# Kernel optimization log

Measured on AMD Instinct MI355X. Metric: run time of the kernel, lower is better.

The kernel has to match this reference:

```python
import jax, jax.numpy as jnp
import numpy as np

B, S, D = 2, 2048, 2048
H, HD = 16, 128
P = 2048  # past (cached) kv length


def setup_inputs() -> dict:
    key = jax.random.key(0)
    ks = jax.random.split(key, 12)
    sw = 1.0 / np.sqrt(D)
    inp = {
        "x": jax.random.normal(ks[0], (B, S, D), jnp.float32),
        "past_k": jax.random.normal(ks[1], (B, H, P, HD), jnp.float32),
        "past_v": jax.random.normal(ks[2], (B, H, P, HD), jnp.float32),
        "Wq": jax.random.normal(ks[3], (D, D), jnp.float32) * sw,
        "bq": jax.random.normal(ks[4], (D,), jnp.float32) * 0.01,
        "Wk": jax.random.normal(ks[5], (D, D), jnp.float32) * sw,
        "bk": jax.random.normal(ks[6], (D,), jnp.float32) * 0.01,
        "Wv": jax.random.normal(ks[7], (D, D), jnp.float32) * sw,
        "bv": jax.random.normal(ks[8], (D,), jnp.float32) * 0.01,
        "Wo": jax.random.normal(ks[9], (D, D), jnp.float32) * sw,
        "bo": jax.random.normal(ks[10], (D,), jnp.float32) * 0.01,
    }
    return inp


def _heads(t):
    # [B, S, D] -> [B, H, S, HD]
    return t.reshape(B, -1, H, HD).transpose(0, 2, 1, 3)


def reference(x, past_k, past_v, Wq, bq, Wk, bk, Wv, bv, Wo, bo):
    # QKV projections (separate weights, _qkv_same_embed_dim=False path)
    q = _heads(x @ Wq.T + bq)          # [B,H,S,HD]
    k_new = _heads(x @ Wk.T + bk)      # [B,H,S,HD]
    v_new = _heads(x @ Wv.T + bv)

    # KV cache append
    k_cached = jnp.concatenate([past_k, k_new], axis=2)  # [B,H,P+S,HD]
    v_cached = jnp.concatenate([past_v, v_new], axis=2)
    cached_len = P + S

    # Manual attention path (query_seq_len != cached_seq_len)
    scale = 1.0 / np.sqrt(HD)
    scores = jnp.einsum('bhqd,bhkd->bhqk', q, k_cached) * scale  # [B,H,S,P+S]
    q_pos = jnp.arange(cached_len - S, cached_len)[:, None]
    k_pos = jnp.arange(cached_len)[None, :]
    mask = q_pos >= k_pos  # offset causal mask [S, P+S]
    scores = jnp.where(mask, scores, -jnp.inf)
    attn = jax.nn.softmax(scores, axis=-1)
    out = jnp.einsum('bhqk,bhkd->bhqd', attn, v_cached)  # [B,H,S,HD]

    out = out.transpose(0, 2, 1, 3).reshape(B, S, D)
    return out @ Wo.T + bo
```

## Files before the change

kernel.cpp:

```cpp
#include <hip/hip_runtime.h>

typedef unsigned short u16;
typedef __attribute__((ext_vector_type(4))) float f32x4;
typedef __attribute__((ext_vector_type(16))) float f32x16;
typedef __attribute__((ext_vector_type(8))) short s16x8;
typedef __attribute__((ext_vector_type(2))) unsigned int u32x2v;

#define CEXP 0.12751742929f

static __device__ __forceinline__ u16 f2bf(float x) {
  unsigned u = __float_as_uint(x);
  u = u + 0x7fffu + ((u >> 16) & 1u);
  return (u16)(u >> 16);
}
static __device__ __forceinline__ unsigned cvtpk(float a, float b) {
  unsigned r;
  asm("v_cvt_pk_bf16_f32 %0, %1, %2" : "=v"(r) : "v"(a), "v"(b));
  return r;
}
static __device__ __forceinline__ u32x2v pswap(unsigned a, unsigned b) {
  return __builtin_amdgcn_permlane32_swap(a, b, false, false);
}
static __device__ __forceinline__ f32x4 fzero() { f32x4 z; z[0]=0.f; z[1]=0.f; z[2]=0.f; z[3]=0.f; return z; }
static __device__ __forceinline__ f32x4 mfma16(s16x8 a, s16x8 b, f32x4 c) {
  return __builtin_amdgcn_mfma_f32_16x16x32_bf16(a, b, c, 0, 0, 0);
}
static __device__ __forceinline__ f32x16 mfma32(s16x8 a, s16x8 b, f32x16 c) {
  return __builtin_amdgcn_mfma_f32_32x32x16_bf16(a, b, c, 0, 0, 0);
}
static __device__ __forceinline__ void gld16(const void* g, void* l) {
  __builtin_amdgcn_global_load_lds((const __attribute__((address_space(1))) void*)g,
                                   (__attribute__((address_space(3))) void*)l, 16, 0, 0);
}

__global__ void cvt_kernel(const float* __restrict__ s, u16* __restrict__ d, int n4, int lg) {
  int stride = gridDim.x * blockDim.x;
  for (int i4 = blockIdx.x * blockDim.x + threadIdx.x; i4 < n4; i4 += stride) {
    int i = i4 * 4;
    float4 v = *reinterpret_cast<const float4*>(s + i);
    size_t di = (size_t)i + ((size_t)(i >> lg) << lg);
    ushort4 o;
    o.x = f2bf(v.x); o.y = f2bf(v.y); o.z = f2bf(v.z); o.w = f2bf(v.w);
    *reinterpret_cast<ushort4*>(d + di) = o;
  }
}

__global__ void transpose_past_v(const float* __restrict__ src, u16* __restrict__ dst) {
  __shared__ u16 tile[64 * 138];
  int bh = blockIdx.y, pt = blockIdx.x;
  const float* s = src + ((size_t)bh * 2048 + (size_t)pt * 64) * 128;
  int t = threadIdx.x;
#pragma unroll
  for (int it = 0; it < 8; ++it) {
    int idx = it * 1024 + t * 4;
    int row = idx >> 7, col = idx & 127;
    float4 v = *reinterpret_cast<const float4*>(s + idx);
    u16* d = &tile[row * 138 + col];
    d[0] = f2bf(v.x); d[1] = f2bf(v.y); d[2] = f2bf(v.z); d[3] = f2bf(v.w);
  }
  __syncthreads();
  size_t dbase = (size_t)bh * 128 * 4096 + (size_t)pt * 64;
#pragma unroll
  for (int it = 0; it < 32; ++it) {
    int o = it * 256 + t;
    int dd = o >> 6, pos = o & 63;
    dst[dbase + (size_t)dd * 4096 + pos] = tile[pos * 138 + dd];
  }
}

__global__ void transpose_new_v(const u16* __restrict__ src, u16* __restrict__ dst) {
  __shared__ u16 tile[64 * 138];
  int bh = blockIdx.y, pt = blockIdx.x;
  const u16* s = src + ((size_t)bh * 2048 + (size_t)pt * 64) * 128;
  int t = threadIdx.x;
#pragma unroll
  for (int it = 0; it < 8; ++it) {
    int idx = it * 1024 + t * 4;
    int row = idx >> 7, col = idx & 127;
    ushort4 v = *reinterpret_cast<const ushort4*>(s + idx);
    u16* d = &tile[row * 138 + col];
    d[0] = v.x; d[1] = v.y; d[2] = v.z; d[3] = v.w;
  }
  __syncthreads();
  size_t dbase = (size_t)bh * 128 * 4096 + 2048 + (size_t)pt * 64;
#pragma unroll
  for (int it = 0; it < 32; ++it) {
    int o = it * 256 + t;
    int dd = o >> 6, pos = o & 63;
    dst[dbase + (size_t)dd * 4096 + pos] = tile[pos * 138 + dd];
  }
}

static __device__ __forceinline__ void gemm_core(const u16* __restrict__ A, const u16* __restrict__ Wn,
                                                 int m0, char* ldsb, f32x4 (&acc)[4][4]) {
  const int tid = threadIdx.x;
  const int w = tid >> 6, lane = tid & 63, g = lane >> 4, ln = lane & 15;
#pragma unroll
  for (int mi = 0; mi < 4; ++mi)
#pragma unroll
    for (int ni = 0; ni < 4; ++ni) acc[mi][ni] = fzero();

  auto stage = [&](int buf, int k0) {
#pragma unroll
    for (int i = 0; i < 2; ++i) {
      int c = w * 2 + i;
      int p = c * 1024 + lane * 16;
      int row = p >> 6;
      int colb = (p & 63) ^ ((row & 3) << 4);
      const u16* sa = A + (size_t)(m0 + row) * 2048 + k0 + (colb >> 1);
      const u16* sw = Wn + (size_t)row * 2048 + k0 + (colb >> 1);
      char* da = ldsb + buf * 16384 + c * 1024;
      gld16(sa, da);
      gld16(sw, da + 8192);
    }
  };
  stage(0, 0);
  __syncthreads();
  const int wr = w >> 1, wc = w & 1;
  for (int kt = 0; kt < 64; ++kt) {
    int cur = kt & 1;
    if (kt < 63) stage(cur ^ 1, (kt + 1) * 32);
    const char* bp = ldsb + cur * 16384;
    s16x8 af[4], bw[4];
#pragma unroll
    for (int mi = 0; mi < 4; ++mi) {
      int row = wr * 64 + mi * 16 + ln;
      int lin = row * 64 + g * 16;
      af[mi] = *reinterpret_cast<const s16x8*>(bp + (lin ^ ((row & 3) << 4)));
    }
#pragma unroll
    for (int ni = 0; ni < 4; ++ni) {
      int row = wc * 64 + ni * 16 + ln;
      int lin = row * 64 + g * 16;
      bw[ni] = *reinterpret_cast<const s16x8*>(bp + 8192 + (lin ^ ((row & 3) << 4)));
    }
#pragma unroll
    for (int mi = 0; mi < 4; ++mi)
#pragma unroll
      for (int ni = 0; ni < 4; ++ni)
        acc[mi][ni] = mfma16(af[mi], bw[ni], acc[mi][ni]);
    __syncthreads();
  }
}

__global__ __launch_bounds__(256, 3) void qkv_gemm(const u16* __restrict__ xb,
    const u16* __restrict__ wq, const u16* __restrict__ wk, const u16* __restrict__ wv,
    const float* __restrict__ bq, const float* __restrict__ bk, const float* __restrict__ bv,
    u16* __restrict__ outq, u16* __restrict__ kc, u16* __restrict__ outv) {
  __shared__ char ldsb[32768];
  int m0 = blockIdx.x * 128;
  int ny = blockIdx.y;
  int wsel = ny >> 4, n0 = (ny & 15) * 128;
  const u16* W; const float* bias; u16* dst; int lrow, off;
  if (wsel == 0)      { W = wq; bias = bq; dst = outq; lrow = 2048; off = 0; }
  else if (wsel == 1) { W = wk; bias = bk; dst = kc;   lrow = 4096; off = 2048; }
  else                { W = wv; bias = bv; dst = outv; lrow = 2048; off = 0; }
  f32x4 acc[4][4];
  gemm_core(xb, W + (size_t)n0 * 2048, m0, ldsb, acc);
  const int tid = threadIdx.x, w = tid >> 6, lane = tid & 63, g = lane >> 4, ln = lane & 15;
  const int wr = w >> 1, wc = w & 1;
#pragma unroll
  for (int ni = 0; ni < 4; ++ni) {
    int j = n0 + wc * 64 + ni * 16 + ln;
    float bcol = bias[j];
    int h = j >> 7, hd = j & 127;
#pragma unroll
    for (int mi = 0; mi < 4; ++mi) {
#pragma unroll
      for (int r = 0; r < 4; ++r) {
        int rowg = m0 + wr * 64 + mi * 16 + g * 4 + r;
        int b = rowg >> 11, s = rowg & 2047;
        float val = acc[mi][ni][r] + bcol;
        dst[((size_t)(b * 16 + h) * lrow + off + s) * 128 + hd] = f2bf(val);
      }
    }
  }
}

__global__ __launch_bounds__(256, 3) void proj_gemm(const u16* __restrict__ ao, const u16* __restrict__ wo,
    const float* __restrict__ bo, float* __restrict__ out) {
  __shared__ char ldsb[32768];
  int m0 = blockIdx.x * 128, n0 = blockIdx.y * 128;
  f32x4 acc[4][4];
  gemm_core(ao, wo + (size_t)n0 * 2048, m0, ldsb, acc);
  const int tid = threadIdx.x, w = tid >> 6, lane = tid & 63, g = lane >> 4, ln = lane & 15;
  const int wr = w >> 1, wc = w & 1;
#pragma unroll
  for (int ni = 0; ni < 4; ++ni) {
    int j = n0 + wc * 64 + ni * 16 + ln;
    float bcol = bo[j];
#pragma unroll
    for (int mi = 0; mi < 4; ++mi) {
#pragma unroll
      for (int r = 0; r < 4; ++r) {
        int rowg = m0 + wr * 64 + mi * 16 + g * 4 + r;
        out[(size_t)rowg * 2048 + j] = acc[mi][ni][r] + bcol;
      }
    }
  }
}

__global__ __launch_bounds__(256, 2) void attn_kernel(const u16* __restrict__ Qb,
    const u16* __restrict__ Kc, const u16* __restrict__ Vt, u16* __restrict__ Ao) {
  __shared__ char lds[65536];
  const int tid = threadIdx.x, w = tid >> 6, lane = tid & 63;
  const int hi = lane >> 5, l5 = lane & 31;
  const int bh = blockIdx.x;
  const int qy = blockIdx.y;
  const int qbk = (qy & 8) ? (15 - (qy & 7)) : qy;
  const int b = bh >> 4, h = bh & 15;
  const u16* Qbh = Qb + (size_t)bh * 2048 * 128;
  const u16* Kbh = Kc + (size_t)bh * 4096 * 128;
  const u16* Vbh = Vt + (size_t)bh * 128 * 4096;

  const int qrow0 = qbk * 128 + w * 32;
  const int qp = 2048 + qrow0 + l5;
  const int qpmin = 2048 + qrow0;
  const int ntiles = (2048 + qbk * 128 + 128) >> 6;

  s16x8 qf[8];
#pragma unroll
  for (int kc = 0; kc < 8; ++kc)
    qf[kc] = *reinterpret_cast<const s16x8*>(Qbh + (size_t)(qrow0 + l5) * 128 + kc * 16 + hi * 8);

  f32x16 o[4];
#pragma unroll
  for (int dt = 0; dt < 4; ++dt)
#pragma unroll
    for (int i = 0; i < 16; ++i) o[dt][i] = 0.f;
  float mrun = -3e38f, lrun = 0.f;

  auto stage = [&](int buf, int kv0) {
    char* base = lds + buf * 32768;
#pragma unroll
    for (int i = 0; i < 4; ++i) {
      int p = (w * 4 + i) * 1024 + lane * 16;
      int row = p >> 8;
      int colb = (p & 255) ^ ((row & 7) << 4);
      gld16(Kbh + (size_t)(kv0 + row) * 128 + (colb >> 1), base + (w * 4 + i) * 1024);
      int vrow = p >> 7;
      int vcol = (p & 127) ^ ((vrow & 7) << 4);
      gld16(Vbh + (size_t)vrow * 4096 + kv0 + (vcol >> 1), base + 16384 + (w * 4 + i) * 1024);
    }
  };

  stage(0, 0);
  for (int t = 0; t < ntiles; ++t) {
    const int kv0 = t * 64;
    const int cur = t & 1;
    if (t + 1 < ntiles) {
      stage(cur ^ 1, kv0 + 64);
      asm volatile("s_waitcnt vmcnt(8)\n\ts_barrier" ::: "memory");
    } else {
      asm volatile("s_waitcnt vmcnt(0)\n\ts_barrier" ::: "memory");
    }
    const char* Kl = lds + cur * 32768;
    const char* Vl = Kl + 16384;
    if (kv0 <= qpmin + 31) {
      f32x16 s0, s1;
#pragma unroll
      for (int i = 0; i < 16; ++i) { s0[i] = 0.f; s1[i] = 0.f; }
      __builtin_amdgcn_s_setprio(1);
#pragma unroll
      for (int kc = 0; kc < 8; ++kc) {
        {
          int row = l5;
          int lin = row * 256 + kc * 32 + hi * 16;
          s16x8 a = *reinterpret_cast<const s16x8*>(Kl + (lin ^ ((row & 7) << 4)));
          s0 = mfma32(a, qf[kc], s0);
        }
        {
          int row = 32 + l5;
          int lin = row * 256 + kc * 32 + hi * 16;
          s16x8 a = *reinterpret_cast<const s16x8*>(Kl + (lin ^ ((row & 7) << 4)));
          s1 = mfma32(a, qf[kc], s1);
        }
      }
      __builtin_amdgcn_s_setprio(0);
      if (kv0 + 63 > qpmin) {
#pragma unroll
        for (int i = 0; i < 16; ++i) {
          int r0 = (i & 3) + 8 * (i >> 2) + 4 * hi;
          if (kv0 + r0 > qp) s0[i] = -3e38f;
          if (kv0 + 32 + r0 > qp) s1[i] = -3e38f;
        }
      }
      float pm = s0[0];
#pragma unroll
      for (int i = 1; i < 16; ++i) pm = fmaxf(pm, s0[i]);
#pragma unroll
      for (int i = 0; i < 16; ++i) pm = fmaxf(pm, s1[i]);
      {
        u32x2v rr = pswap(__float_as_uint(pm), __float_as_uint(pm));
        pm = fmaxf(pm, __uint_as_float(hi ? rr[0] : rr[1]));
      }
      float mnew = (pm > mrun + 8.f) ? pm : mrun;
      float fsc = exp2f((mrun - mnew) * CEXP);
      mrun = mnew;
      float rs = 0.f;
#pragma unroll
      for (int i = 0; i < 16; ++i) { float p = exp2f((s0[i] - mnew) * CEXP); s0[i] = p; rs += p; }
#pragma unroll
      for (int i = 0; i < 16; ++i) { float p = exp2f((s1[i] - mnew) * CEXP); s1[i] = p; rs += p; }
      {
        u32x2v rr = pswap(__float_as_uint(rs), __float_as_uint(rs));
        rs += __uint_as_float(hi ? rr[0] : rr[1]);
      }
      lrun = lrun * fsc + rs;
      if (!__all(fsc == 1.f)) {
#pragma unroll
        for (int dt = 0; dt < 4; ++dt)
#pragma unroll
          for (int i = 0; i < 16; ++i) o[dt][i] *= fsc;
      }
      s16x8 pb[4];
#pragma unroll
      for (int c2 = 0; c2 < 4; ++c2) {
        const f32x16& sv = (c2 & 2) ? s1 : s0;
        const int b0 = (c2 & 1) * 8;
        unsigned x0 = cvtpk(sv[b0 + 0], sv[b0 + 1]);
        unsigned x1 = cvtpk(sv[b0 + 2], sv[b0 + 3]);
        unsigned y0 = cvtpk(sv[b0 + 4], sv[b0 + 5]);
        unsigned y1 = cvtpk(sv[b0 + 6], sv[b0 + 7]);
        u32x2v r0 = pswap(x0, y0);
        u32x2v r1 = pswap(x1, y1);
        union { unsigned u[4]; s16x8 v; } pu;
        pu.u[0] = r0[0]; pu.u[1] = r1[0]; pu.u[2] = r0[1]; pu.u[3] = r1[1];
        pb[c2] = pu.v;
      }
      __builtin_amdgcn_s_setprio(1);
#pragma unroll
      for (int dt = 0; dt < 4; ++dt) {
#pragma unroll
        for (int c2 = 0; c2 < 4; ++c2) {
          int row = dt * 32 + l5;
          int lin = row * 128 + c2 * 32 + hi * 16;
          s16x8 va = *reinterpret_cast<const s16x8*>(Vl + (lin ^ ((row & 7) << 4)));
          o[dt] = mfma32(va, pb[c2], o[dt]);
        }
      }
      __builtin_amdgcn_s_setprio(0);
    }
    asm volatile("s_waitcnt lgkmcnt(0)\n\ts_barrier" ::: "memory");
  }

  float li = 1.f / lrun;
#pragma unroll
  for (int dt = 0; dt < 4; ++dt)
#pragma unroll
    for (int i = 0; i < 16; ++i) o[dt][i] *= li;
  const int qb = w * 32 + l5;
#pragma unroll
  for (int dt = 0; dt < 4; ++dt) {
#pragma unroll
    for (int rg = 0; rg < 4; ++rg) {
      int d0 = dt * 32 + rg * 8 + hi * 4;
      unsigned w0 = cvtpk(o[dt][rg * 4 + 0], o[dt][rg * 4 + 1]);
      unsigned w1 = cvtpk(o[dt][rg * 4 + 2], o[dt][rg * 4 + 3]);
      int lin = qb * 256 + d0 * 2;
      int phys = lin ^ ((qb & 7) << 4);
      *reinterpret_cast<uint2*>(lds + phys) = make_uint2(w0, w1);
    }
  }
  __syncthreads();
  const int qr = tid >> 4, c16 = tid & 15;
#pragma unroll
  for (int it = 0; it < 8; ++it) {
    int q = qr + it * 16;
    int phys = (q * 256 + c16 * 16) ^ ((q & 7) << 4);
    s16x8 v = *reinterpret_cast<const s16x8*>(lds + phys);
    *reinterpret_cast<s16x8*>(Ao + ((size_t)(b * 2048 + qbk * 128 + q)) * 2048 + h * 128 + c16 * 8) = v;
  }
}

extern "C" void kernel_launch(void* const* d_in, const int* in_sizes, int n_in,
                              void* d_out, int out_size, void* d_ws, size_t ws_size,
                              hipStream_t stream) {
  const float* x      = (const float*)d_in[0];
  const float* past_k = (const float*)d_in[1];
  const float* past_v = (const float*)d_in[2];
  const float* Wq = (const float*)d_in[3];
  const float* bq = (const float*)d_in[4];
  const float* Wk = (const float*)d_in[5];
  const float* bk = (const float*)d_in[6];
  const float* Wv = (const float*)d_in[7];
  const float* bv = (const float*)d_in[8];
  const float* Wo = (const float*)d_in[9];
  const float* bo = (const float*)d_in[10];
  float* out = (float*)d_out;

  char* ws = (char*)d_ws;
  u16* xb   = (u16*)(ws);
  u16* wqb  = (u16*)(ws + 16777216);
  u16* wkb  = (u16*)(ws + 25165824);
  u16* wvb  = (u16*)(ws + 33554432);
  u16* wob  = (u16*)(ws + 41943040);
  u16* kc   = (u16*)(ws + 50331648);
  u16* qbuf = (u16*)(ws + 83886080);
  u16* vn   = (u16*)(ws + 100663296);
  u16* vt   = (u16*)(ws + 117440512);
  u16* ao   = xb;

  cvt_kernel<<<1024, 256, 0, stream>>>(x, xb, 2097152, 30);
  cvt_kernel<<<1024, 256, 0, stream>>>(Wq, wqb, 1048576, 30);
  cvt_kernel<<<1024, 256, 0, stream>>>(Wk, wkb, 1048576, 30);
  cvt_kernel<<<1024, 256, 0, stream>>>(Wv, wvb, 1048576, 30);
  cvt_kernel<<<1024, 256, 0, stream>>>(Wo, wob, 1048576, 30);
  cvt_kernel<<<1024, 256, 0, stream>>>(past_k, kc, 2097152, 18);
  transpose_past_v<<<dim3(32, 32), 256, 0, stream>>>(past_v, vt);
  qkv_gemm<<<dim3(32, 48), 256, 0, stream>>>(xb, wqb, wkb, wvb, bq, bk, bv, qbuf, kc, vn);
  transpose_new_v<<<dim3(32, 32), 256, 0, stream>>>(vn, vt);
  attn_kernel<<<dim3(32, 16), 256, 0, stream>>>(qbuf, kc, vt, ao);
  proj_gemm<<<dim3(32, 16), 256, 0, stream>>>(ao, wob, bo, out);
}
```

Baseline: 390.5 us.

## Overlap GEMM loads with compute and single-buffer V in attention

The GEMM core's full __syncthreads is replaced by explicit partial vmcnt waits, so the prefetch of the next K-tile can stay in flight while the current tile is consumed. In attention, K stays double-buffered but V is single-buffered, and its next tile is loaded after the end-of-iteration barrier. This cuts LDS to 48KB and allows 3 blocks per CU instead of 2. The max and exp-sum reductions are also split into independent chains for more instruction-level parallelism, at the cost of V load latency being less hidden and more register pressure at the higher occupancy target.

```diff
diff --git a/kernel.cpp b/kernel.cpp
--- a/kernel.cpp
+++ b/kernel.cpp
@@ -115,11 +115,15 @@
     }
   };
   stage(0, 0);
-  __syncthreads();
   const int wr = w >> 1, wc = w & 1;
   for (int kt = 0; kt < 64; ++kt) {
     int cur = kt & 1;
-    if (kt < 63) stage(cur ^ 1, (kt + 1) * 32);
+    if (kt < 63) {
+      stage(cur ^ 1, (kt + 1) * 32);
+      asm volatile("s_waitcnt vmcnt(4)\n\ts_barrier" ::: "memory");
+    } else {
+      asm volatile("s_waitcnt vmcnt(0)\n\ts_barrier" ::: "memory");
+    }
     const char* bp = ldsb + cur * 16384;
     s16x8 af[4], bw[4];
 #pragma unroll
@@ -139,7 +143,7 @@
 #pragma unroll
       for (int ni = 0; ni < 4; ++ni)
         acc[mi][ni] = mfma16(af[mi], bw[ni], acc[mi][ni]);
-    __syncthreads();
+    asm volatile("s_waitcnt lgkmcnt(0)\n\ts_barrier" ::: "memory");
   }
 }
 
@@ -200,9 +204,9 @@
   }
 }
 
-__global__ __launch_bounds__(256, 2) void attn_kernel(const u16* __restrict__ Qb,
+__global__ __launch_bounds__(256, 3) void attn_kernel(const u16* __restrict__ Qb,
     const u16* __restrict__ Kc, const u16* __restrict__ Vt, u16* __restrict__ Ao) {
-  __shared__ char lds[65536];
+  __shared__ char lds[49152];
   const int tid = threadIdx.x, w = tid >> 6, lane = tid & 63;
   const int hi = lane >> 5, l5 = lane & 31;
   const int bh = blockIdx.x;
@@ -230,32 +234,40 @@
     for (int i = 0; i < 16; ++i) o[dt][i] = 0.f;
   float mrun = -3e38f, lrun = 0.f;
 
-  auto stage = [&](int buf, int kv0) {
-    char* base = lds + buf * 32768;
+  auto stageK = [&](int buf, int kv0) {
+    char* base = lds + buf * 16384;
 #pragma unroll
     for (int i = 0; i < 4; ++i) {
       int p = (w * 4 + i) * 1024 + lane * 16;
       int row = p >> 8;
       int colb = (p & 255) ^ ((row & 7) << 4);
       gld16(Kbh + (size_t)(kv0 + row) * 128 + (colb >> 1), base + (w * 4 + i) * 1024);
+    }
+  };
+  auto stageV = [&](int kv0) {
+    char* base = lds + 32768;
+#pragma unroll
+    for (int i = 0; i < 4; ++i) {
+      int p = (w * 4 + i) * 1024 + lane * 16;
       int vrow = p >> 7;
       int vcol = (p & 127) ^ ((vrow & 7) << 4);
-      gld16(Vbh + (size_t)vrow * 4096 + kv0 + (vcol >> 1), base + 16384 + (w * 4 + i) * 1024);
+      gld16(Vbh + (size_t)vrow * 4096 + kv0 + (vcol >> 1), base + (w * 4 + i) * 1024);
     }
   };
 
-  stage(0, 0);
+  stageK(0, 0);
+  stageV(0);
   for (int t = 0; t < ntiles; ++t) {
     const int kv0 = t * 64;
     const int cur = t & 1;
     if (t + 1 < ntiles) {
-      stage(cur ^ 1, kv0 + 64);
-      asm volatile("s_waitcnt vmcnt(8)\n\ts_barrier" ::: "memory");
+      stageK(cur ^ 1, kv0 + 64);
+      asm volatile("s_waitcnt vmcnt(4)\n\ts_barrier" ::: "memory");
     } else {
       asm volatile("s_waitcnt vmcnt(0)\n\ts_barrier" ::: "memory");
     }
-    const char* Kl = lds + cur * 32768;
-    const char* Vl = Kl + 16384;
+    const char* Kl = lds + cur * 16384;
+    const char* Vl = lds + 32768;
     if (kv0 <= qpmin + 31) {
       f32x16 s0, s1;
 #pragma unroll
@@ -285,11 +297,11 @@
           if (kv0 + 32 + r0 > qp) s1[i] = -3e38f;
         }
       }
-      float pm = s0[0];
-#pragma unroll
-      for (int i = 1; i < 16; ++i) pm = fmaxf(pm, s0[i]);
-#pragma unroll
-      for (int i = 0; i < 16; ++i) pm = fmaxf(pm, s1[i]);
+      float pm = fmaxf(s0[0], s0[1]);
+#pragma unroll
+      for (int i = 2; i < 16; i += 2) pm = fmaxf(fmaxf(pm, s0[i]), s0[i + 1]);
+#pragma unroll
+      for (int i = 0; i < 16; i += 2) pm = fmaxf(fmaxf(pm, s1[i]), s1[i + 1]);
       {
         u32x2v rr = pswap(__float_as_uint(pm), __float_as_uint(pm));
         pm = fmaxf(pm, __uint_as_float(hi ? rr[0] : rr[1]));
@@ -297,11 +309,26 @@
       float mnew = (pm > mrun + 8.f) ? pm : mrun;
       float fsc = exp2f((mrun - mnew) * CEXP);
       mrun = mnew;
-      float rs = 0.f;
-#pragma unroll
-      for (int i = 0; i < 16; ++i) { float p = exp2f((s0[i] - mnew) * CEXP); s0[i] = p; rs += p; }
-#pragma unroll
-      for (int i = 0; i < 16; ++i) { float p = exp2f((s1[i] - mnew) * CEXP); s1[i] = p; rs += p; }
+      float r0 = 0.f, r1 = 0.f, r2 = 0.f, r3 = 0.f;
+#pragma unroll
+      for (int i = 0; i < 16; i += 4) {
+        float p0 = exp2f((s0[i] - mnew) * CEXP);
+        float p1 = exp2f((s0[i + 1] - mnew) * CEXP);
+        float p2 = exp2f((s0[i + 2] - mnew) * CEXP);
+        float p3 = exp2f((s0[i + 3] - mnew) * CEXP);
+        s0[i] = p0; s0[i + 1] = p1; s0[i + 2] = p2; s0[i + 3] = p3;
+        r0 += p0; r1 += p1; r2 += p2; r3 += p3;
+      }
+#pragma unroll
+      for (int i = 0; i < 16; i += 4) {
+        float p0 = exp2f((s1[i] - mnew) * CEXP);
+        float p1 = exp2f((s1[i + 1] - mnew) * CEXP);
+        float p2 = exp2f((s1[i + 2] - mnew) * CEXP);
+        float p3 = exp2f((s1[i + 3] - mnew) * CEXP);
+        s1[i] = p0; s1[i + 1] = p1; s1[i + 2] = p2; s1[i + 3] = p3;
+        r0 += p0; r1 += p1; r2 += p2; r3 += p3;
+      }
+      float rs = (r0 + r1) + (r2 + r3);
       {
         u32x2v rr = pswap(__float_as_uint(rs), __float_as_uint(rs));
         rs += __uint_as_float(hi ? rr[0] : rr[1]);
@@ -322,10 +349,10 @@
         unsigned x1 = cvtpk(sv[b0 + 2], sv[b0 + 3]);
         unsigned y0 = cvtpk(sv[b0 + 4], sv[b0 + 5]);
         unsigned y1 = cvtpk(sv[b0 + 6], sv[b0 + 7]);
-        u32x2v r0 = pswap(x0, y0);
-        u32x2v r1 = pswap(x1, y1);
+        u32x2v q0 = pswap(x0, y0);
+        u32x2v q1 = pswap(x1, y1);
         union { unsigned u[4]; s16x8 v; } pu;
-        pu.u[0] = r0[0]; pu.u[1] = r1[0]; pu.u[2] = r0[1]; pu.u[3] = r1[1];
+        pu.u[0] = q0[0]; pu.u[1] = q1[0]; pu.u[2] = q0[1]; pu.u[3] = q1[1];
         pb[c2] = pu.v;
       }
       __builtin_amdgcn_s_setprio(1);
@@ -342,6 +369,7 @@
       __builtin_amdgcn_s_setprio(0);
     }
     asm volatile("s_waitcnt lgkmcnt(0)\n\ts_barrier" ::: "memory");
+    if (t + 1 < ntiles) stageV(kv0 + 64);
   }
 
   float li = 1.f / lrun;
```

After: 519.1 us. 1.33x slower.
